# Performance work log

Measured on AMD Instinct MI355X. Metric: run time of the kernel, lower is better.

The kernel has to match this reference:

```python
import jax, jax.numpy as jnp
import numpy as np

N, E, D_IN, HID, HEADS, OUT = 20000, 320000, 256, 128, 2, 4

def _gatv2(x, src, dst, Wl, Wr, att, b, n_nodes):
    # GATv2Conv (PyG defaults): lin_l on source, lin_r on target,
    # e_ij = att . leaky_relu(xl_j + xr_i), softmax over incoming edges of i,
    # out_i = sum_j alpha_ij * xl_j, heads concatenated, plus bias.
    H, C = att.shape
    xl = (x @ Wl).reshape(-1, H, C)  # [N,H,C] source transform
    xr = (x @ Wr).reshape(-1, H, C)  # [N,H,C] target transform
    m = jax.nn.leaky_relu(xl[src] + xr[dst], 0.2)          # [E,H,C]
    e = jnp.einsum('ehc,hc->eh', m, att)                    # [E,H]
    emax = jax.ops.segment_max(e, dst, num_segments=n_nodes)
    ex = jnp.exp(e - emax[dst])
    denom = jax.ops.segment_sum(ex, dst, num_segments=n_nodes)
    alpha = ex / denom[dst]                                 # [E,H]
    out = jax.ops.segment_sum(alpha[:, :, None] * xl[src], dst, num_segments=n_nodes)
    return out.reshape(n_nodes, H * C) + b

def _glorot(key, shape, scale=0.05):
    return jax.random.normal(key, shape, dtype=jnp.float32) * scale

def setup_inputs() -> dict:
    key = jax.random.key(0)
    ks = jax.random.split(key, 20)
    inp = {
        'x': jax.random.normal(ks[0], (N, D_IN), dtype=jnp.float32),
        'edge_index': jax.random.randint(ks[1], (2, E), 0, N, dtype=jnp.int64),
    }
    dims = [D_IN, HID * HEADS, HID * HEADS]
    k = 2
    for li, din in enumerate(dims, start=1):
        inp[f'Wl{li}'] = _glorot(ks[k], (din, HEADS * HID)); k += 1
        inp[f'Wr{li}'] = _glorot(ks[k], (din, HEADS * HID)); k += 1
        inp[f'att{li}'] = _glorot(ks[k], (HEADS, HID)); k += 1
        inp[f'b{li}'] = jnp.zeros((HEADS * HID,), dtype=jnp.float32)
    inp['Wout'] = _glorot(ks[k], (HEADS * HID, OUT)); k += 1
    inp['bout'] = jnp.zeros((OUT,), dtype=jnp.float32)
    return inp

def reference(x, edge_index, Wl1, Wr1, att1, b1, Wl2, Wr2, att2, b2,
              Wl3, Wr3, att3, b3, Wout, bout):
    n = x.shape[0]
    # add_self_loops=True (PyG default)
    loops = jnp.arange(n, dtype=edge_index.dtype)
    ei = jnp.concatenate([edge_index, jnp.stack([loops, loops])], axis=1)
    src, dst = ei[0], ei[1]
    h = jax.nn.relu(_gatv2(x, src, dst, Wl1, Wr1, att1, b1, n))
    h = jax.nn.relu(_gatv2(h, src, dst, Wl2, Wr2, att2, b2, n))
    h = jax.nn.relu(_gatv2(h, src, dst, Wl3, Wr3, att3, b3, n))
    return h @ Wout + bout
```

## Files before the change

kernel.cpp:

```cpp
#include <hip/hip_runtime.h>
#include <hip/hip_bf16.h>
#include <hip/hip_fp16.h>
#include <math.h>

#define NCH 256
#define LEAKY 0.2f

typedef __attribute__((ext_vector_type(8))) _Float16 half8_t;
typedef __attribute__((ext_vector_type(2))) _Float16 half2_t;
typedef __attribute__((ext_vector_type(4))) float f32x4;

static __device__ __forceinline__ half2_t u2h2(unsigned u) {
    return __builtin_bit_cast(half2_t, u);
}

static __device__ __forceinline__ void f32_to_hl8(const float4 a, const float4 b,
                                                  uint4& h, uint4& l) {
    float f[8] = {a.x, a.y, a.z, a.w, b.x, b.y, b.z, b.w};
    unsigned hs[8], ls[8];
    #pragma unroll
    for (int c = 0; c < 8; ++c) {
        __half hh = __float2half_rn(f[c]);
        hs[c] = __half_as_ushort(hh);
        ls[c] = __half_as_ushort(__float2half_rn(f[c] - __half2float(hh)));
    }
    h = make_uint4(hs[0] | (hs[1] << 16), hs[2] | (hs[3] << 16),
                   hs[4] | (hs[5] << 16), hs[6] | (hs[7] << 16));
    l = make_uint4(ls[0] | (ls[1] << 16), ls[2] | (ls[3] << 16),
                   ls[4] | (ls[5] << 16), ls[6] | (ls[7] << 16));
}

__global__ void zero_kernel(int* __restrict__ p, int n) {
    int i = blockIdx.x * 256 + threadIdx.x;
    if (i < n) p[i] = 0;
}

__global__ void count_kernel(const int* __restrict__ ei, int E, int n,
                             int* __restrict__ counts) {
    int tid = blockIdx.x * 256 + threadIdx.x;
    int E4 = E >> 2;
    if (tid < E4) {
        int4 d = ((const int4*)(ei + E))[tid];
        atomicAdd(&counts[d.x], 1);
        atomicAdd(&counts[d.y], 1);
        atomicAdd(&counts[d.z], 1);
        atomicAdd(&counts[d.w], 1);
    } else {
        int s = tid - E4;
        if (s < n) atomicAdd(&counts[s], 1);
    }
}

__global__ void scan_kernel(const int* __restrict__ counts,
                            int* __restrict__ offsets,
                            int* __restrict__ cursor, int n) {
    __shared__ int wsum[16];
    int tid  = threadIdx.x;
    int lane = tid & 63, w = tid >> 6;
    int carry = 0;
    for (int base = 0; base < n; base += 4096) {
        int i0 = base + tid * 4;
        int v0 = 0, v1 = 0, v2 = 0, v3 = 0;
        if (i0 + 3 < n) {
            int4 v = *(const int4*)&counts[i0];
            v0 = v.x; v1 = v.y; v2 = v.z; v3 = v.w;
        } else if (i0 < n) {
            v0 = counts[i0];
            if (i0 + 1 < n) v1 = counts[i0 + 1];
            if (i0 + 2 < n) v2 = counts[i0 + 2];
        }
        int c1 = v0 + v1, c2 = c1 + v2, c3 = c2 + v3;
        int tsum = c3;
        int incl = tsum;
        #pragma unroll
        for (int off = 1; off < 64; off <<= 1) {
            int t2 = __shfl_up(incl, off, 64);
            if (lane >= off) incl += t2;
        }
        if (lane == 63) wsum[w] = incl;
        __syncthreads();
        if (w == 0 && lane < 16) {
            int s = wsum[lane];
            #pragma unroll
            for (int off = 1; off < 16; off <<= 1) {
                int t2 = __shfl_up(s, off, 64);
                if (lane >= off) s += t2;
            }
            wsum[lane] = s;
        }
        __syncthreads();
        int wpre = (w == 0) ? 0 : wsum[w - 1];
        int excl = carry + wpre + incl - tsum;
        if (i0 + 3 < n) {
            int4 o = make_int4(excl, excl + v0, excl + c1, excl + c2);
            *(int4*)&offsets[i0] = o;
            *(int4*)&cursor[i0]  = o;
        } else if (i0 < n) {
            offsets[i0] = excl;           cursor[i0] = excl;
            if (i0 + 1 < n) { offsets[i0 + 1] = excl + v0; cursor[i0 + 1] = excl + v0; }
            if (i0 + 2 < n) { offsets[i0 + 2] = excl + c1; cursor[i0 + 2] = excl + c1; }
        }
        carry += wsum[15];
        __syncthreads();
    }
    if (tid == 0) offsets[n] = carry;
}

__global__ void scatter_kernel(const int* __restrict__ ei, int E, int n,
                               int* __restrict__ cursor,
                               int* __restrict__ csr_src) {
    int tid = blockIdx.x * 256 + threadIdx.x;
    int E4 = E >> 2;
    if (tid < E4) {
        int4 s = ((const int4*)ei)[tid];
        int4 d = ((const int4*)(ei + E))[tid];
        csr_src[atomicAdd(&cursor[d.x], 1)] = s.x;
        csr_src[atomicAdd(&cursor[d.y], 1)] = s.y;
        csr_src[atomicAdd(&cursor[d.z], 1)] = s.z;
        csr_src[atomicAdd(&cursor[d.w], 1)] = s.w;
    } else {
        int i = tid - E4;
        if (i < n) csr_src[atomicAdd(&cursor[i], 1)] = i;
    }
}

struct WPtrs { const float* w[6]; };
__global__ __launch_bounds__(1024) void wsplit_kernel(WPtrs p,
        __half* __restrict__ wt) {
    __shared__ float tile[32][33];
    int m = blockIdx.z;
    const float* W = p.w[m];
    size_t base = (size_t)m * 65536;
    int k = blockIdx.y * 32 + threadIdx.y;
    int n = blockIdx.x * 32 + threadIdx.x;
    tile[threadIdx.y][threadIdx.x] = W[k * NCH + n];
    __syncthreads();
    int on = blockIdx.x * 32 + threadIdx.y;
    int ok = blockIdx.y * 32 + threadIdx.x;
    wt[base + (size_t)on * NCH + ok] = __float2half_rn(tile[threadIdx.x][threadIdx.y]);
}

#define LDK 40
template <int AF32>
__global__ __launch_bounds__(256) void dual_gemm_mfma(
        const float* __restrict__ Af,
        const __half* __restrict__ Ahi, const __half* __restrict__ Alo,
        const __half* __restrict__ Bt,
        __half* __restrict__ xlh, float* __restrict__ xr, int M) {
    __shared__ ushort As[2][128 * LDK];
    __shared__ ushort Bs[128 * LDK];
    int b = blockIdx.x;
    int stripe = b >> 5;
    int wslot  = b & 31;
    int rt = (stripe << 3) + (wslot & 7);
    int cb = wslot >> 3;
    int row0 = rt * 128;
    if (row0 >= M) return;
    const __half* Bm = Bt + (size_t)(cb >> 1) * 65536;
    int col0 = (cb & 1) * 128;
    int t = threadIdx.x;
    int lane = t & 63, w = t >> 6;
    int wr = w >> 1, wc = w & 1;
    int l15 = lane & 15, l4 = lane >> 4;

    f32x4 acc[4][4];
    #pragma unroll
    for (int i = 0; i < 4; ++i)
        #pragma unroll
        for (int j = 0; j < 4; ++j) acc[i][j] = (f32x4){0.f, 0.f, 0.f, 0.f};

    int r0 = t >> 2,          q0 = (t & 3) * 8;
    int r1 = (t + 256) >> 2,  q1 = ((t + 256) & 3) * 8;

    for (int k0 = 0; k0 < 256; k0 += 32) {
        uint4 z = make_uint4(0, 0, 0, 0);
        uint4 a0h = z, a0l = z, a1h = z, a1l = z;
        if (row0 + r0 < M) {
            if (AF32) {
                float4 fa = *(const float4*)&Af[(size_t)(row0 + r0) * NCH + k0 + q0];
                float4 fb = *(const float4*)&Af[(size_t)(row0 + r0) * NCH + k0 + q0 + 4];
                f32_to_hl8(fa, fb, a0h, a0l);
            } else {
                a0h = *(const uint4*)&Ahi[(size_t)(row0 + r0) * NCH + k0 + q0];
                a0l = *(const uint4*)&Alo[(size_t)(row0 + r0) * NCH + k0 + q0];
            }
        }
        if (row0 + r1 < M) {
            if (AF32) {
                float4 fa = *(const float4*)&Af[(size_t)(row0 + r1) * NCH + k0 + q1];
                float4 fb = *(const float4*)&Af[(size_t)(row0 + r1) * NCH + k0 + q1 + 4];
                f32_to_hl8(fa, fb, a1h, a1l);
            } else {
                a1h = *(const uint4*)&Ahi[(size_t)(row0 + r1) * NCH + k0 + q1];
                a1l = *(const uint4*)&Alo[(size_t)(row0 + r1) * NCH + k0 + q1];
            }
        }
        uint4 b0 = *(const uint4*)&Bm[(size_t)(col0 + r0) * NCH + k0 + q0];
        uint4 b1 = *(const uint4*)&Bm[(size_t)(col0 + r1) * NCH + k0 + q1];
        __syncthreads();
        *(uint4*)&As[0][r0 * LDK + q0] = a0h;
        *(uint4*)&As[1][r0 * LDK + q0] = a0l;
        *(uint4*)&As[0][r1 * LDK + q1] = a1h;
        *(uint4*)&As[1][r1 * LDK + q1] = a1l;
        *(uint4*)&Bs[r0 * LDK + q0] = b0;
        *(uint4*)&Bs[r1 * LDK + q1] = b1;
        __syncthreads();

        half8_t af[4][2], bq[4];
        #pragma unroll
        for (int fm = 0; fm < 4; ++fm) {
            int addr = (wr * 64 + fm * 16 + l15) * LDK + l4 * 8;
            af[fm][0] = *(const half8_t*)&As[0][addr];
            af[fm][1] = *(const half8_t*)&As[1][addr];
        }
        #pragma unroll
        for (int fn = 0; fn < 4; ++fn) {
            int addr = (wc * 64 + fn * 16 + l15) * LDK + l4 * 8;
            bq[fn] = *(const half8_t*)&Bs[addr];
        }
        #pragma unroll
        for (int fm = 0; fm < 4; ++fm)
            #pragma unroll
            for (int fn = 0; fn < 4; ++fn) {
                acc[fm][fn] = __builtin_amdgcn_mfma_f32_16x16x32_f16(
                    af[fm][0], bq[fn], acc[fm][fn], 0, 0, 0);
                acc[fm][fn] = __builtin_amdgcn_mfma_f32_16x16x32_f16(
                    af[fm][1], bq[fn], acc[fm][fn], 0, 0, 0);
            }
    }

    #pragma unroll
    for (int fm = 0; fm < 4; ++fm)
        #pragma unroll
        for (int fn = 0; fn < 4; ++fn) {
            int col = col0 + wc * 64 + fn * 16 + l15;
            #pragma unroll
            for (int r = 0; r < 4; ++r) {
                int row = row0 + wr * 64 + fm * 16 + l4 * 4 + r;
                if (row < M) {
                    if (cb < 2)
                        xlh[(size_t)row * NCH + col] = __float2half_rn(acc[fm][fn][r]);
                    else
                        xr[(size_t)row * NCH + col] = acc[fm][fn][r];
                }
            }
        }
}

static __device__ __forceinline__ float edge_dot(
        const uint4& r, const half2_t* xrh, const half2_t* atth) {
    const half2_t zh = (half2_t){(_Float16)0.f, (_Float16)0.f};
    const half2_t ch = (half2_t){(_Float16)LEAKY, (_Float16)LEAKY};
    float p = 0.f;
    #pragma unroll
    for (int q = 0; q < 4; ++q) {
        unsigned u = (&r.x)[q];
        half2_t t = u2h2(u) + xrh[q];
        half2_t m = __builtin_elementwise_max(t, zh) +
                    ch * __builtin_elementwise_min(t, zh);
        p = __builtin_amdgcn_fdot2(m, atth[q], p, false);
    }
    return p;
}

template <int LAST>
__global__ __launch_bounds__(256) void gat_agg8(
        const __half* __restrict__ xlh, const float* __restrict__ xr,
        const float* __restrict__ att, const float* __restrict__ bias,
        const int* __restrict__ offsets, const int* __restrict__ csr_src,
        __half* __restrict__ hhi, __half* __restrict__ hlo,
        const float* __restrict__ Wout, const float* __restrict__ bout,
        float* __restrict__ out, int nNodes) {
    int wid  = threadIdx.x >> 6;
    int lane = threadIdx.x & 63;
    int el = lane >> 5;
    int l  = lane & 31;
    int c0 = l * 8;

    half2_t atth[4];
    {
        float a8[8];
        *(float4*)&a8[0] = *(const float4*)&att[c0];
        *(float4*)&a8[4] = *(const float4*)&att[c0 + 4];
        #pragma unroll
        for (int q = 0; q < 4; ++q)
            atth[q] = (half2_t){(_Float16)a8[2 * q], (_Float16)a8[2 * q + 1]};
    }

    int stride = gridDim.x << 2;
    for (int node0 = (blockIdx.x << 2) + wid; node0 < nNodes; node0 += stride) {
        int node = __builtin_amdgcn_readfirstlane(node0);
        half2_t xrh[4];
        {
            float x8[8];
            *(float4*)&x8[0] = *(const float4*)&xr[(size_t)node * NCH + c0];
            *(float4*)&x8[4] = *(const float4*)&xr[(size_t)node * NCH + c0 + 4];
            #pragma unroll
            for (int q = 0; q < 4; ++q)
                xrh[q] = (half2_t){(_Float16)x8[2 * q], (_Float16)x8[2 * q + 1]};
        }

        int begin = offsets[node], end = offsets[node + 1];
        float denom = 0.f;
        float acc8[8];
        #pragma unroll
        for (int c = 0; c < 8; ++c) acc8[c] = 0.f;

        for (int j = begin; j < end; j += 4) {
            int j1 = j + 1 < end ? j + 1 : end - 1;
            int j2 = j + 2 < end ? j + 2 : end - 1;
            int j3 = j + 3 < end ? j + 3 : end - 1;
            int i0 = csr_src[j];
            int i1 = csr_src[j1];
            int i2 = csr_src[j2];
            int i3 = csr_src[j3];
            int sA = el ? i1 : i0;
            int sB = el ? i3 : i2;
            uint4 rA = *(const uint4*)&xlh[(size_t)sA * NCH + c0];
            uint4 rB = *(const uint4*)&xlh[(size_t)sB * NCH + c0];

            float pA = edge_dot(rA, xrh, atth);
            float pB = edge_dot(rB, xrh, atth);
            #pragma unroll
            for (int off = 1; off < 16; off <<= 1) {
                pA += __shfl_xor(pA, off);
                pB += __shfl_xor(pB, off);
            }
            float exA = (j + el < end)     ? __expf(pA) : 0.f;
            float exB = (j + 2 + el < end) ? __expf(pB) : 0.f;
            denom += exA + exB;
            #pragma unroll
            for (int q = 0; q < 4; ++q) {
                float2 fa = __half22float2(*(const __half2*)&(&rA.x)[q]);
                float2 fb = __half22float2(*(const __half2*)&(&rB.x)[q]);
                acc8[2 * q]     = fmaf(exA, fa.x, acc8[2 * q]);
                acc8[2 * q + 1] = fmaf(exA, fa.y, acc8[2 * q + 1]);
                acc8[2 * q]     = fmaf(exB, fb.x, acc8[2 * q]);
                acc8[2 * q + 1] = fmaf(exB, fb.y, acc8[2 * q + 1]);
            }
        }

        #pragma unroll
        for (int c = 0; c < 8; ++c) acc8[c] += __shfl_xor(acc8[c], 32);
        denom += __shfl_xor(denom, 32);
        float rd = 1.0f / denom;

        float o8[8], bi8[8];
        *(float4*)&bi8[0] = *(const float4*)&bias[c0];
        *(float4*)&bi8[4] = *(const float4*)&bias[c0 + 4];
        #pragma unroll
        for (int c = 0; c < 8; ++c)
            o8[c] = fmaxf(fmaf(acc8[c], rd, bi8[c]), 0.f);

        if (!LAST) {
            if (el == 0) {
                ushort h8[8], lo8[8];
                #pragma unroll
                for (int c = 0; c < 8; ++c) {
                    __half h = __float2half_rn(o8[c]);
                    h8[c]  = __half_as_ushort(h);
                    lo8[c] = __half_as_ushort(__float2half_rn(o8[c] - __half2float(h)));
                }
                *(uint4*)&hhi[(size_t)node * NCH + c0] = *(uint4*)&h8[0];
                *(uint4*)&hlo[(size_t)node * NCH + c0] = *(uint4*)&lo8[0];
            }
        } else {
            float p0 = 0.f, p1 = 0.f, p2 = 0.f, p3 = 0.f;
            #pragma unroll
            for (int c = 0; c < 8; ++c) {
                float4 w4 = *(const float4*)&Wout[(size_t)(c0 + c) * 4];
                p0 = fmaf(o8[c], w4.x, p0);
                p1 = fmaf(o8[c], w4.y, p1);
                p2 = fmaf(o8[c], w4.z, p2);
                p3 = fmaf(o8[c], w4.w, p3);
            }
            #pragma unroll
            for (int off = 1; off < 32; off <<= 1) {
                p0 += __shfl_xor(p0, off);
                p1 += __shfl_xor(p1, off);
                p2 += __shfl_xor(p2, off);
                p3 += __shfl_xor(p3, off);
            }
            if (lane == 0) {
                float4 r;
                r.x = p0 + bout[0]; r.y = p1 + bout[1];
                r.z = p2 + bout[2]; r.w = p3 + bout[3];
                *(float4*)&out[(size_t)node * 4] = r;
            }
        }
    }
}

extern "C" void kernel_launch(void* const* d_in, const int* in_sizes, int n_in,
                              void* d_out, int out_size, void* d_ws, size_t ws_size,
                              hipStream_t stream) {
    const float* x  = (const float*)d_in[0];
    const int*   ei = (const int*)d_in[1];
    const float* Wl[3]  = {(const float*)d_in[2], (const float*)d_in[6],  (const float*)d_in[10]};
    const float* Wr[3]  = {(const float*)d_in[3], (const float*)d_in[7],  (const float*)d_in[11]};
    const float* att[3] = {(const float*)d_in[4], (const float*)d_in[8],  (const float*)d_in[12]};
    const float* bb[3]  = {(const float*)d_in[5], (const float*)d_in[9],  (const float*)d_in[13]};
    const float* Wout = (const float*)d_in[14];
    const float* bout = (const float*)d_in[15];

    int Nn   = in_sizes[0] / NCH;
    int E    = in_sizes[1] / 2;

    size_t NEf = (size_t)Nn * NCH;
    __half* xlh  = (__half*)d_ws;
    float*  xr   = (float*)(xlh + NEf);
    __half* bAhi = (__half*)(xr + NEf);
    __half* bAlo = bAhi + NEf;
    __half* bBhi = bAlo + NEf;
    __half* bBlo = bBhi + NEf;
    __half* wt   = bBlo + NEf;
    int*   counts  = (int*)(wt + 6 * 65536);
    int*   offsets = counts + Nn;
    int*   cursor  = offsets + (Nn + 1);
    int*   csr_src = cursor + Nn;

    zero_kernel<<<(Nn + 255) / 256, 256, 0, stream>>>(counts, Nn);
    int vthreads = (E >> 2) + Nn;
    int vblocks  = (vthreads + 255) / 256;
    count_kernel<<<vblocks, 256, 0, stream>>>(ei, E, Nn, counts);
    scan_kernel<<<1, 1024, 0, stream>>>(counts, offsets, cursor, Nn);
    scatter_kernel<<<vblocks, 256, 0, stream>>>(ei, E, Nn, cursor, csr_src);

    WPtrs wp = {{Wl[0], Wr[0], Wl[1], Wr[1], Wl[2], Wr[2]}};
    wsplit_kernel<<<dim3(8, 8, 6), dim3(32, 32), 0, stream>>>(wp, wt);

    int nrt = (Nn + 127) / 128;
    int prt = ((nrt + 7) / 8) * 8;
    int gblocks = prt * 4;
    int nblocks = 2048;
    if (nblocks > (Nn + 3) / 4) nblocks = (Nn + 3) / 4;

    dual_gemm_mfma<1><<<gblocks, 256, 0, stream>>>(x, nullptr, nullptr,
                                                   wt, xlh, xr, Nn);
    gat_agg8<0><<<nblocks, 256, 0, stream>>>(xlh, xr, att[0], bb[0],
        offsets, csr_src, bAhi, bAlo, nullptr, nullptr, nullptr, Nn);
    dual_gemm_mfma<0><<<gblocks, 256, 0, stream>>>(nullptr, bAhi, bAlo,
                                                   wt + 2 * 65536, xlh, xr, Nn);
    gat_agg8<0><<<nblocks, 256, 0, stream>>>(xlh, xr, att[1], bb[1],
        offsets, csr_src, bBhi, bBlo, nullptr, nullptr, nullptr, Nn);
    dual_gemm_mfma<0><<<gblocks, 256, 0, stream>>>(nullptr, bBhi, bBlo,
                                                   wt + 4 * 65536, xlh, xr, Nn);
    gat_agg8<1><<<nblocks, 256, 0, stream>>>(xlh, xr, att[2], bb[2],
        offsets, csr_src, nullptr, nullptr, Wout, bout, (float*)d_out, Nn);
}
```

Measured before the change: 212.0 us.

## Process two nodes per wave in GAT aggregation and read GEMM B fragments directly

The aggregation kernel now gives each wave exactly two destination nodes, handled in one interleaved loop, instead of a grid-stride loop over single nodes. The goal is more gathers in flight per wave to hide the latency of the random xl row loads, at the cost of more registers and wasted work when the two degrees differ. Separately, the dual GEMM no longer stages the weight tile in shared memory; each wave loads its B fragments straight from global memory (expected to hit cache). That drops the shared-memory traffic for B but adds redundant global loads.

Result: slower. 224.3 us (+5.8%).

```diff
diff --git a/kernel.cpp b/kernel.cpp
--- a/kernel.cpp
+++ b/kernel.cpp
@@ -148,7 +148,6 @@
         const __half* __restrict__ Bt,
         __half* __restrict__ xlh, float* __restrict__ xr, int M) {
     __shared__ ushort As[2][128 * LDK];
-    __shared__ ushort Bs[128 * LDK];
     int b = blockIdx.x;
     int stripe = b >> 5;
     int wslot  = b & 31;
@@ -195,28 +194,23 @@
                 a1l = *(const uint4*)&Alo[(size_t)(row0 + r1) * NCH + k0 + q1];
             }
         }
-        uint4 b0 = *(const uint4*)&Bm[(size_t)(col0 + r0) * NCH + k0 + q0];
-        uint4 b1 = *(const uint4*)&Bm[(size_t)(col0 + r1) * NCH + k0 + q1];
         __syncthreads();
         *(uint4*)&As[0][r0 * LDK + q0] = a0h;
         *(uint4*)&As[1][r0 * LDK + q0] = a0l;
         *(uint4*)&As[0][r1 * LDK + q1] = a1h;
         *(uint4*)&As[1][r1 * LDK + q1] = a1l;
-        *(uint4*)&Bs[r0 * LDK + q0] = b0;
-        *(uint4*)&Bs[r1 * LDK + q1] = b1;
         __syncthreads();
 
         half8_t af[4][2], bq[4];
+        #pragma unroll
+        for (int fn = 0; fn < 4; ++fn)
+            bq[fn] = *(const half8_t*)&Bm[(size_t)(col0 + wc * 64 + fn * 16 + l15) * NCH
+                                          + k0 + l4 * 8];
         #pragma unroll
         for (int fm = 0; fm < 4; ++fm) {
             int addr = (wr * 64 + fm * 16 + l15) * LDK + l4 * 8;
             af[fm][0] = *(const half8_t*)&As[0][addr];
             af[fm][1] = *(const half8_t*)&As[1][addr];
-        }
-        #pragma unroll
-        for (int fn = 0; fn < 4; ++fn) {
-            int addr = (wc * 64 + fn * 16 + l15) * LDK + l4 * 8;
-            bq[fn] = *(const half8_t*)&Bs[addr];
         }
         #pragma unroll
         for (int fm = 0; fm < 4; ++fm)
@@ -264,7 +258,7 @@
 }
 
 template <int LAST>
-__global__ __launch_bounds__(256) void gat_agg8(
+__global__ __launch_bounds__(256) void gat_agg9(
         const __half* __restrict__ xlh, const float* __restrict__ xr,
         const float* __restrict__ att, const float* __restrict__ bias,
         const int* __restrict__ offsets, const int* __restrict__ csr_src,
@@ -287,106 +281,175 @@
             atth[q] = (half2_t){(_Float16)a8[2 * q], (_Float16)a8[2 * q + 1]};
     }
 
-    int stride = gridDim.x << 2;
-    for (int node0 = (blockIdx.x << 2) + wid; node0 < nNodes; node0 += stride) {
-        int node = __builtin_amdgcn_readfirstlane(node0);
-        half2_t xrh[4];
-        {
-            float x8[8];
-            *(float4*)&x8[0] = *(const float4*)&xr[(size_t)node * NCH + c0];
-            *(float4*)&x8[4] = *(const float4*)&xr[(size_t)node * NCH + c0 + 4];
+    int gw = __builtin_amdgcn_readfirstlane(blockIdx.x * 4 + wid);
+    int n0 = gw * 2;
+    if (n0 >= nNodes) return;
+    int n1 = n0 + 1;
+    bool has1 = n1 < nNodes;
+    int n1s = has1 ? n1 : n0;
+
+    half2_t xrh0[4], xrh1[4];
+    {
+        float x8[8];
+        *(float4*)&x8[0] = *(const float4*)&xr[(size_t)n0 * NCH + c0];
+        *(float4*)&x8[4] = *(const float4*)&xr[(size_t)n0 * NCH + c0 + 4];
+        #pragma unroll
+        for (int q = 0; q < 4; ++q)
+            xrh0[q] = (half2_t){(_Float16)x8[2 * q], (_Float16)x8[2 * q + 1]};
+        *(float4*)&x8[0] = *(const float4*)&xr[(size_t)n1s * NCH + c0];
+        *(float4*)&x8[4] = *(const float4*)&xr[(size_t)n1s * NCH + c0 + 4];
+        #pragma unroll
+        for (int q = 0; q < 4; ++q)
+            xrh1[q] = (half2_t){(_Float16)x8[2 * q], (_Float16)x8[2 * q + 1]};
+    }
+
+    int b0 = offsets[n0], e0 = offsets[n0 + 1];
+    int b1 = b0, e1 = b0;
+    if (has1) { b1 = e0; e1 = offsets[n1 + 1]; }
+    int len0 = e0 - b0, len1 = e1 - b1;
+    int lmax = len0 > len1 ? len0 : len1;
+
+    float den0 = 0.f, den1 = 0.f;
+    float acc0[8], acc1[8];
+    #pragma unroll
+    for (int c = 0; c < 8; ++c) { acc0[c] = 0.f; acc1[c] = 0.f; }
+
+    for (int o = 0; o < lmax; o += 4) {
+        int j0 = b0 + o, j1 = b1 + o;
+        int e0m = e0 - 1, e1m = e1 > b1 ? e1 - 1 : b1;
+        int i00 = csr_src[j0     < e0m ? j0     : e0m];
+        int i01 = csr_src[j0 + 1 < e0m ? j0 + 1 : e0m];
+        int i02 = csr_src[j0 + 2 < e0m ? j0 + 2 : e0m];
+        int i03 = csr_src[j0 + 3 < e0m ? j0 + 3 : e0m];
+        int i10 = csr_src[j1     < e1m ? j1     : e1m];
+        int i11 = csr_src[j1 + 1 < e1m ? j1 + 1 : e1m];
+        int i12 = csr_src[j1 + 2 < e1m ? j1 + 2 : e1m];
+        int i13 = csr_src[j1 + 3 < e1m ? j1 + 3 : e1m];
+        int sA0 = el ? i01 : i00;
+        int sB0 = el ? i03 : i02;
+        int sA1 = el ? i11 : i10;
+        int sB1 = el ? i13 : i12;
+        uint4 rA0 = *(const uint4*)&xlh[(size_t)sA0 * NCH + c0];
+        uint4 rB0 = *(const uint4*)&xlh[(size_t)sB0 * NCH + c0];
+        uint4 rA1 = *(const uint4*)&xlh[(size_t)sA1 * NCH + c0];
+        uint4 rB1 = *(const uint4*)&xlh[(size_t)sB1 * NCH + c0];
+
+        float pA0 = edge_dot(rA0, xrh0, atth);
+        float pB0 = edge_dot(rB0, xrh0, atth);
+        float pA1 = edge_dot(rA1, xrh1, atth);
+        float pB1 = edge_dot(rB1, xrh1, atth);
+        #pragma unroll
+        for (int off = 1; off < 16; off <<= 1) {
+            pA0 += __shfl_xor(pA0, off);
+            pB0 += __shfl_xor(pB0, off);
+            pA1 += __shfl_xor(pA1, off);
+            pB1 += __shfl_xor(pB1, off);
+        }
+        float exA0 = (j0 + el < e0)     ? __expf(pA0) : 0.f;
+        float exB0 = (j0 + 2 + el < e0) ? __expf(pB0) : 0.f;
+        float exA1 = (j1 + el < e1)     ? __expf(pA1) : 0.f;
+        float exB1 = (j1 + 2 + el < e1) ? __expf(pB1) : 0.f;
+        den0 += exA0 + exB0;
+        den1 += exA1 + exB1;
+        #pragma unroll
+        for (int q = 0; q < 4; ++q) {
+            float2 fa = __half22float2(*(const __half2*)&(&rA0.x)[q]);
+            float2 fb = __half22float2(*(const __half2*)&(&rB0.x)[q]);
+            acc0[2 * q]     = fmaf(exA0, fa.x, acc0[2 * q]);
+            acc0[2 * q + 1] = fmaf(exA0, fa.y, acc0[2 * q + 1]);
+            acc0[2 * q]     = fmaf(exB0, fb.x, acc0[2 * q]);
+            acc0[2 * q + 1] = fmaf(exB0, fb.y, acc0[2 * q + 1]);
+        }
+        #pragma unroll
+        for (int q = 0; q < 4; ++q) {
+            float2 fa = __half22float2(*(const __half2*)&(&rA1.x)[q]);
+            float2 fb = __half22float2(*(const __half2*)&(&rB1.x)[q]);
+            acc1[2 * q]     = fmaf(exA1, fa.x, acc1[2 * q]);
+            acc1[2 * q + 1] = fmaf(exA1, fa.y, acc1[2 * q + 1]);
+            acc1[2 * q]     = fmaf(exB1, fb.x, acc1[2 * q]);
+            acc1[2 * q + 1] = fmaf(exB1, fb.y, acc1[2 * q + 1]);
+        }
+    }
+
+    #pragma unroll
+    for (int c = 0; c < 8; ++c) {
+        acc0[c] += __shfl_xor(acc0[c], 32);
+        acc1[c] += __shfl_xor(acc1[c], 32);
+    }
+    den0 += __shfl_xor(den0, 32);
+    den1 += __shfl_xor(den1, 32);
+    float rd0 = 1.0f / den0;
+    float rd1 = 1.0f / den1;
+
+    float bi8[8];
+    *(float4*)&bi8[0] = *(const float4*)&bias[c0];
+    *(float4*)&bi8[4] = *(const float4*)&bias[c0 + 4];
+    float o0[8], o1[8];
+    #pragma unroll
+    for (int c = 0; c < 8; ++c) {
+        o0[c] = fmaxf(fmaf(acc0[c], rd0, bi8[c]), 0.f);
+        o1[c] = fmaxf(fmaf(acc1[c], rd1, bi8[c]), 0.f);
+    }
+
+    if (!LAST) {
+        if (el == 0) {
+            ushort h8[8], lo8[8];
             #pragma unroll
-            for (int q = 0; q < 4; ++q)
-                xrh[q] = (half2_t){(_Float16)x8[2 * q], (_Float16)x8[2 * q + 1]};
-        }
-
-        int begin = offsets[node], end = offsets[node + 1];
-        float denom = 0.f;
-        float acc8[8];
-        #pragma unroll
-        for (int c = 0; c < 8; ++c) acc8[c] = 0.f;
-
-        for (int j = begin; j < end; j += 4) {
-            int j1 = j + 1 < end ? j + 1 : end - 1;
-            int j2 = j + 2 < end ? j + 2 : end - 1;
-            int j3 = j + 3 < end ? j + 3 : end - 1;
-            int i0 = csr_src[j];
-            int i1 = csr_src[j1];
-            int i2 = csr_src[j2];
-            int i3 = csr_src[j3];
-            int sA = el ? i1 : i0;
-            int sB = el ? i3 : i2;
-            uint4 rA = *(const uint4*)&xlh[(size_t)sA * NCH + c0];
-            uint4 rB = *(const uint4*)&xlh[(size_t)sB * NCH + c0];
-
-            float pA = edge_dot(rA, xrh, atth);
-            float pB = edge_dot(rB, xrh, atth);
-            #pragma unroll
-            for (int off = 1; off < 16; off <<= 1) {
-                pA += __shfl_xor(pA, off);
-                pB += __shfl_xor(pB, off);
-            }
-            float exA = (j + el < end)     ? __expf(pA) : 0.f;
-            float exB = (j + 2 + el < end) ? __expf(pB) : 0.f;
-            denom += exA + exB;
-            #pragma unroll
-            for (int q = 0; q < 4; ++q) {
-                float2 fa = __half22float2(*(const __half2*)&(&rA.x)[q]);
-                float2 fb = __half22float2(*(const __half2*)&(&rB.x)[q]);
-                acc8[2 * q]     = fmaf(exA, fa.x, acc8[2 * q]);
-                acc8[2 * q + 1] = fmaf(exA, fa.y, acc8[2 * q + 1]);
-                acc8[2 * q]     = fmaf(exB, fb.x, acc8[2 * q]);
-                acc8[2 * q + 1] = fmaf(exB, fb.y, acc8[2 * q + 1]);
-            }
-        }
-
-        #pragma unroll
-        for (int c = 0; c < 8; ++c) acc8[c] += __shfl_xor(acc8[c], 32);
-        denom += __shfl_xor(denom, 32);
-        float rd = 1.0f / denom;
-
-        float o8[8], bi8[8];
-        *(float4*)&bi8[0] = *(const float4*)&bias[c0];
-        *(float4*)&bi8[4] = *(const float4*)&bias[c0 + 4];
-        #pragma unroll
-        for (int c = 0; c < 8; ++c)
-            o8[c] = fmaxf(fmaf(acc8[c], rd, bi8[c]), 0.f);
-
-        if (!LAST) {
-            if (el == 0) {
-                ushort h8[8], lo8[8];
+            for (int c = 0; c < 8; ++c) {
+                __half h = __float2half_rn(o0[c]);
+                h8[c]  = __half_as_ushort(h);
+                lo8[c] = __half_as_ushort(__float2half_rn(o0[c] - __half2float(h)));
+            }
+            *(uint4*)&hhi[(size_t)n0 * NCH + c0] = *(uint4*)&h8[0];
+            *(uint4*)&hlo[(size_t)n0 * NCH + c0] = *(uint4*)&lo8[0];
+            if (has1) {
                 #pragma unroll
                 for (int c = 0; c < 8; ++c) {
-                    __half h = __float2half_rn(o8[c]);
+                    __half h = __float2half_rn(o1[c]);
                     h8[c]  = __half_as_ushort(h);
-                    lo8[c] = __half_as_ushort(__float2half_rn(o8[c] - __half2float(h)));
+                    lo8[c] = __half_as_ushort(__float2half_rn(o1[c] - __half2float(h)));
                 }
-                *(uint4*)&hhi[(size_t)node * NCH + c0] = *(uint4*)&h8[0];
-                *(uint4*)&hlo[(size_t)node * NCH + c0] = *(uint4*)&lo8[0];
-            }
-        } else {
-            float p0 = 0.f, p1 = 0.f, p2 = 0.f, p3 = 0.f;
-            #pragma unroll
-            for (int c = 0; c < 8; ++c) {
-                float4 w4 = *(const float4*)&Wout[(size_t)(c0 + c) * 4];
-                p0 = fmaf(o8[c], w4.x, p0);
-                p1 = fmaf(o8[c], w4.y, p1);
-                p2 = fmaf(o8[c], w4.z, p2);
-                p3 = fmaf(o8[c], w4.w, p3);
-            }
-            #pragma unroll
-            for (int off = 1; off < 32; off <<= 1) {
-                p0 += __shfl_xor(p0, off);
-                p1 += __shfl_xor(p1, off);
-                p2 += __shfl_xor(p2, off);
-                p3 += __shfl_xor(p3, off);
-            }
-            if (lane == 0) {
-                float4 r;
-                r.x = p0 + bout[0]; r.y = p1 + bout[1];
-                r.z = p2 + bout[2]; r.w = p3 + bout[3];
-                *(float4*)&out[(size_t)node * 4] = r;
-            }
+                *(uint4*)&hhi[(size_t)n1 * NCH + c0] = *(uint4*)&h8[0];
+                *(uint4*)&hlo[(size_t)n1 * NCH + c0] = *(uint4*)&lo8[0];
+            }
+        }
+    } else {
+        float p0 = 0.f, p1 = 0.f, p2 = 0.f, p3 = 0.f;
+        float q0 = 0.f, q1 = 0.f, q2 = 0.f, q3 = 0.f;
+        #pragma unroll
+        for (int c = 0; c < 8; ++c) {
+            float4 w4 = *(const float4*)&Wout[(size_t)(c0 + c) * 4];
+            p0 = fmaf(o0[c], w4.x, p0);
+            p1 = fmaf(o0[c], w4.y, p1);
+            p2 = fmaf(o0[c], w4.z, p2);
+            p3 = fmaf(o0[c], w4.w, p3);
+            q0 = fmaf(o1[c], w4.x, q0);
+            q1 = fmaf(o1[c], w4.y, q1);
+            q2 = fmaf(o1[c], w4.z, q2);
+            q3 = fmaf(o1[c], w4.w, q3);
+        }
+        #pragma unroll
+        for (int off = 1; off < 32; off <<= 1) {
+            p0 += __shfl_xor(p0, off);
+            p1 += __shfl_xor(p1, off);
+            p2 += __shfl_xor(p2, off);
+            p3 += __shfl_xor(p3, off);
+            q0 += __shfl_xor(q0, off);
+            q1 += __shfl_xor(q1, off);
+            q2 += __shfl_xor(q2, off);
+            q3 += __shfl_xor(q3, off);
+        }
+        if (lane == 0) {
+            float4 r;
+            r.x = p0 + bout[0]; r.y = p1 + bout[1];
+            r.z = p2 + bout[2]; r.w = p3 + bout[3];
+            *(float4*)&out[(size_t)n0 * 4] = r;
+        }
+        if (lane == 32 && has1) {
+            float4 r;
+            r.x = q0 + bout[0]; r.y = q1 + bout[1];
+            r.z = q2 + bout[2]; r.w = q3 + bout[3];
+            *(float4*)&out[(size_t)n1 * 4] = r;
         }
     }
 }
@@ -432,19 +495,18 @@
     int nrt = (Nn + 127) / 128;
     int prt = ((nrt + 7) / 8) * 8;
     int gblocks = prt * 4;
-    int nblocks = 2048;
-    if (nblocks > (Nn + 3) / 4) nblocks = (Nn + 3) / 4;
+    int nblocks = (Nn + 7) / 8;
 
     dual_gemm_mfma<1><<<gblocks, 256, 0, stream>>>(x, nullptr, nullptr,
                                                    wt, xlh, xr, Nn);
-    gat_agg8<0><<<nblocks, 256, 0, stream>>>(xlh, xr, att[0], bb[0],
+    gat_agg9<0><<<nblocks, 256, 0, stream>>>(xlh, xr, att[0], bb[0],
         offsets, csr_src, bAhi, bAlo, nullptr, nullptr, nullptr, Nn);
     dual_gemm_mfma<0><<<gblocks, 256, 0, stream>>>(nullptr, bAhi, bAlo,
                                                    wt + 2 * 65536, xlh, xr, Nn);
-    gat_agg8<0><<<nblocks, 256, 0, stream>>>(xlh, xr, att[1], bb[1],
+    gat_agg9<0><<<nblocks, 256, 0, stream>>>(xlh, xr, att[1], bb[1],
         offsets, csr_src, bBhi, bBlo, nullptr, nullptr, nullptr, Nn);
     dual_gemm_mfma<0><<<gblocks, 256, 0, stream>>>(nullptr, bBhi, bBlo,
                                                    wt + 4 * 65536, xlh, xr, Nn);
-    gat_agg8<1><<<nblocks, 256, 0, stream>>>(xlh, xr, att[2], bb[2],
+    gat_agg9<1><<<nblocks, 256, 0, stream>>>(xlh, xr, att[2], bb[2],
         offsets, csr_src, nullptr, nullptr, Wout, bout, (float*)d_out, Nn);
 }
```
